# Kernel tuning notes

Measured on AMD Instinct MI355X. Metric: run time of the kernel, lower is better.

## Reference

```python
import jax, jax.numpy as jnp
import numpy as np
import itertools

LLR_MAX = 100.0


def _get_dist(llr, c_hat):
    # llr: [bs, n]; c_hat: [bs, cand, n] -> [bs, cand]
    # LLR-based distance from Stimming et al.: mean_n log(1 + exp(llr * (1 - 2c)))
    x = llr[:, None, :] * (1.0 - 2.0 * c_hat)
    return jnp.mean(jnp.log1p(jnp.exp(x)), axis=2)


def _int_mod_2(x):
    return jnp.mod(jnp.round(x), 2.0)


def _find_mrb(gm):
    # Batched GF(2) Gaussian elimination to most-reliable-basis.
    # gm: [bs, k, n] of 0/1 floats -> (gm_mrb [bs,k,n] systematic, idx_mrb [bs,n])
    bs, k, n = gm.shape

    def step(g, i):
        row = jax.lax.dynamic_slice_in_dim(g, i, 1, axis=1)[:, 0, :]   # [bs, n]
        p = jnp.argmax(row, axis=-1)                                   # first 1 -> pivot col, [bs]
        col = jnp.take_along_axis(g, p[:, None, None], axis=2)[:, :, 0]  # pivot column, [bs, k]
        col = col * (1.0 - jax.nn.one_hot(i, k, dtype=g.dtype))[None, :]  # don't eliminate row i itself
        g = jnp.mod(g + col[:, :, None] * row[:, None, :], 2.0)        # GF(2) row additions
        return g, p

    gm, pivots = jax.lax.scan(step, gm, jnp.arange(k))
    pivots = pivots.T.astype(jnp.int32)                                # [bs, k]
    # non-pivot columns, in original order, go to the back
    mark = jnp.zeros((bs, n), dtype=jnp.int32).at[jnp.arange(bs)[:, None], pivots].set(1)
    idx_parity = jnp.argsort(mark, axis=-1)[:, : n - k].astype(jnp.int32)  # stable: zeros (non-pivots) first
    idx_mrb = jnp.concatenate([pivots, idx_parity], axis=1)            # [bs, n]
    gm_mrb = jnp.take_along_axis(gm, idx_mrb[:, None, :], axis=2)      # systematic [I | P]
    return gm_mrb, idx_mrb


def _find_min_dist(llr, ep, gm_mrb, c):
    # ep: [P, t] error index patterns over the k MRB positions
    e = gm_mrb[:, ep, :]                       # [bs, P, t, n]
    e = jnp.sum(e, axis=2) + c[:, None, :]     # flip t rows of gm onto base codeword
    c_cand = _int_mod_2(e)                     # [bs, P, n]
    d = _get_dist(llr, c_cand)                 # [bs, P]
    idx = jnp.argmin(d, axis=1)
    c_hat = jnp.take_along_axis(c_cand, idx[:, None, None], axis=1)[:, 0, :]
    d_min = jnp.take_along_axis(d, idx[:, None], axis=1)[:, 0]
    return d_min, c_hat


def setup_inputs() -> dict:
    k, n, bs = 64, 128, 128
    rng = np.random.default_rng(0)
    # random systematic generator matrix [I_k | P] (already in the form make_systematic produces)
    P = rng.integers(0, 2, size=(k, n - k))
    gm = jnp.asarray(np.concatenate([np.eye(k, dtype=np.int64), P], axis=1), dtype=jnp.float32)
    key = jax.random.key(0)
    llrs_ch = 2.0 * jax.random.normal(key, (bs, n), dtype=jnp.float32)
    return {"llrs_ch": llrs_ch, "gm": gm, "t": 2}


def reference(llrs_ch, gm, t):
    llr = jnp.clip(llrs_ch, -LLR_MAX, LLR_MAX)
    bs, n = llr.shape
    k = gm.shape[0]
    # 1. sort by reliability |llr| (descending), permute gm columns identically
    idx_sort = jnp.argsort(-jnp.abs(llr), axis=-1).astype(jnp.int32)   # [bs, n]
    llr_sort = jnp.take_along_axis(llr, idx_sort, axis=1)
    gm_b = jnp.broadcast_to(gm[None], (bs, k, n))
    gm_sort = jnp.take_along_axis(gm_b, idx_sort[:, None, :], axis=2)
    # 2. most reliable basis via GF(2) Gaussian elimination
    gm_mrb, idx_mrb = _find_mrb(gm_sort)
    llr_mrb = jnp.take_along_axis(llr_sort, idx_mrb, axis=1)
    idx_total = jnp.take_along_axis(idx_sort, idx_mrb, axis=1)         # composed permutation
    # 3. hard-decide k most reliable bits and re-encode
    u_hat = (llr_mrb[:, :k] > 0.0).astype(llr.dtype)
    c = _int_mod_2(jnp.einsum('bk,bkn->bn', u_hat, gm_mrb))
    d_best = _get_dist(llr_mrb, c[:, None, :])[:, 0]
    c_best = c
    # 4. brute-force search over all error patterns with up to t flips
    for t_i in range(1, int(t) + 1):
        ep = jnp.asarray(list(itertools.combinations(range(k), t_i)), dtype=jnp.int32)
        d, c_hat = _find_min_dist(llr_mrb, ep, gm_mrb, c)
        better = d < d_best
        c_best = jnp.where(better[:, None], c_hat, c_best)
        d_best = jnp.where(better, d, d_best)
    # undo total column permutation
    idx_inv = jnp.argsort(idx_total, axis=-1)
    return jnp.take_along_axis(c_best, idx_inv, axis=1)
```

## Files before the change

kernel.cpp:

```cpp
#include <hip/hip_runtime.h>
#include <stdint.h>

#define K 64
#define N 128
#define BS 128
#define NPAIRS 2016
#define NCAND (64 + NPAIRS)
#define BLOCK 256

typedef unsigned long long u64;
typedef unsigned int u32;

__device__ inline u64 bcast64(u64 v, int lane) {
    int lo = __builtin_amdgcn_readlane((int)(u32)v, lane);
    int hi = __builtin_amdgcn_readlane((int)(u32)(v >> 32), lane);
    return ((u64)(u32)hi << 32) | (u32)lo;
}

__device__ inline int nth_set_bit(u64 m, int i) {
    int pos = 0;
#pragma unroll
    for (int w = 32; w >= 1; w >>= 1) {
        u64 mask = (1ull << w) - 1ull;
        int c = __popcll(m & mask);
        if (i >= c) { i -= c; m >>= w; pos += w; }
    }
    return pos;
}

__global__ __launch_bounds__(BLOCK) void osd_kernel(const float* __restrict__ llrs,
                                                    const float* __restrict__ gm,
                                                    float* __restrict__ out) {
    __shared__ float  lam[N];
    __shared__ u64    skey[N];
    __shared__ int    keyIdx[N];
    __shared__ float  lamSort[N];
    __shared__ u64    gmcols[N];
    __shared__ u64    cols[N];
    __shared__ int    pivotsLds[K];
    __shared__ int    idxpLds[K];
    __shared__ int    markLds[N];
    __shared__ u64    PmaskLds[K];
    __shared__ float  absMrb[K];
    __shared__ double sigLds[K];
    __shared__ double table[8 * 256];
    __shared__ double redS[4];
    __shared__ int    redId[4];
    __shared__ u64    cScal[4];

    const int tid = threadIdx.x;
    const int item = blockIdx.x;
    const float* llr = llrs + item * N;

    if (tid < N) {
        float v = llr[tid];
        v = fminf(fmaxf(v, -100.0f), 100.0f);
        lam[tid] = v;
        u32 ab = __float_as_uint(fabsf(v));
        skey[tid] = ((u64)(0xFFFFFFFFu - ab) << 32) | (u32)tid;
    }
    {
        int col = tid & 127, rh = tid >> 7;
        u32 w = 0;
#pragma unroll
        for (int i = 0; i < 32; ++i)
            w |= (u32)(gm[(rh * 32 + i) * N + col] != 0.0f) << i;
        ((u32*)gmcols)[col * 2 + rh] = w;
    }
    __syncthreads();

    if (tid < 64) {
        for (int k2 = 2; k2 <= N; k2 <<= 1) {
            for (int j = k2 >> 1; j >= 1; j >>= 1) {
                int i = ((tid & ~(j - 1)) << 1) | (tid & (j - 1));
                int ip = i | j;
                u64 a = skey[i], b = skey[ip];
                bool asc = ((i & k2) == 0);
                bool sw = asc ? (a > b) : (a < b);
                if (sw) { skey[i] = b; skey[ip] = a; }
            }
        }
        {
            u64 kv = skey[tid];      int ix = (int)(u32)kv;
            keyIdx[tid] = ix;        lamSort[tid] = lam[ix];
            kv = skey[tid + 64];     ix = (int)(u32)kv;
            keyIdx[tid + 64] = ix;   lamSort[tid + 64] = lam[ix];
        }

        u64 c0 = gmcols[keyIdx[tid]];
        u64 c1 = gmcols[keyIdx[tid + 64]];
        int pivotReg = 0;
        for (int i = 0; i < K; ++i) {
            int b0 = (int)((c0 >> i) & 1ull);
            int b1 = (int)((c1 >> i) & 1ull);
            u64 m0 = __ballot(b0);
            u64 m1 = __ballot(b1);
            int p = m0 ? __builtin_ctzll(m0) : (m1 ? 64 + __builtin_ctzll(m1) : 0);
            u64 colp = (p < 64) ? bcast64(c0, p & 63) : bcast64(c1, p & 63);
            u64 msk = colp & ~(1ull << i);
            if (b0) c0 ^= msk;
            if (b1) c1 ^= msk;
            pivotReg = (i == tid) ? p : pivotReg;
        }
        cols[tid] = c0;
        cols[tid + 64] = c1;
        pivotsLds[tid] = pivotReg;

        markLds[tid] = 0; markLds[tid + 64] = 0;
        markLds[pivotReg] = 1;
        u64 pm0 = __ballot(markLds[tid] != 0);
        u64 pm1 = __ballot(markLds[tid + 64] != 0);
        u64 nm0 = ~pm0, nm1 = ~pm1;
        int c0n = __popcll(nm0);
        int idxpReg = (tid < c0n) ? nth_set_bit(nm0, tid)
                                  : 64 + nth_set_bit(nm1, tid - c0n);
        idxpLds[tid] = idxpReg;

        u64 cp = cols[idxpReg];
        u64 P = 0;
#pragma unroll
        for (int x = 0; x < 64; ++x) {
            u64 bx = __ballot((int)((cp >> x) & 1ull));
            P = (x == tid) ? bx : P;
        }
        PmaskLds[tid] = P;

        float lpv = lamSort[pivotReg];
        int uh = lpv > 0.0f;
        absMrb[tid] = fabsf(lpv);
        u64 cLo = __ballot(uh);
        u64 x = uh ? P : 0ull;
#pragma unroll
        for (int off = 32; off >= 1; off >>= 1) x ^= __shfl_xor(x, off);
        u64 cHi = x;

        float lp = lamSort[idxpReg];
        int cbit = (int)((cHi >> tid) & 1ull);
        sigLds[tid] = cbit ? -(double)lp : (double)lp;

        if (tid == 0) { cScal[0] = cLo; cScal[1] = cHi; }
    }
    __syncthreads();

    {
        int pos = tid >> 5, grp = tid & 31;
        double sg[8];
#pragma unroll
        for (int j = 0; j < 8; ++j) sg[j] = sigLds[pos * 8 + j];
        int g = grp << 3;
        double base = 0.0;
#pragma unroll
        for (int j = 3; j < 8; ++j) if ((g >> j) & 1) base += sg[j];
#pragma unroll
        for (int e = 0; e < 8; ++e) {
            double s = base;
            if (e & 1) s += sg[0];
            if (e & 2) s += sg[1];
            if (e & 4) s += sg[2];
            table[pos * 256 + g + e] = s;
        }
    }
    __syncthreads();

    double bestS = 0.0; int bestId = 0;
    for (int c = tid; c < NCAND; c += BLOCK) {
        u64 mask; double pen; int id;
        if (c < 64) {
            mask = PmaskLds[c];
            pen = (double)absMrb[c];
            id = 1 + c;
        } else {
            int pid = c - 64;
            int lo = 0, hi = 62;
            while (lo < hi) {
                int mid = (lo + hi + 1) >> 1;
                int o = mid * 63 - ((mid * (mid - 1)) >> 1);
                if (o <= pid) lo = mid; else hi = mid - 1;
            }
            int a = lo;
            int oa = a * 63 - ((a * (a - 1)) >> 1);
            int b = a + 1 + (pid - oa);
            mask = PmaskLds[a] ^ PmaskLds[b];
            pen = (double)absMrb[a] + (double)absMrb[b];
            id = 65 + pid;
        }
        double W = 0.0;
#pragma unroll
        for (int p2 = 0; p2 < 8; ++p2)
            W += table[p2 * 256 + (int)((mask >> (p2 * 8)) & 255ull)];
        double s = W - pen;
        if (s > bestS || (s == bestS && id < bestId)) { bestS = s; bestId = id; }
    }
#pragma unroll
    for (int off = 32; off >= 1; off >>= 1) {
        double s2 = __shfl_xor(bestS, off);
        int i2 = __shfl_xor(bestId, off);
        if (s2 > bestS || (s2 == bestS && i2 < bestId)) { bestS = s2; bestId = i2; }
    }
    if ((tid & 63) == 0) { redS[tid >> 6] = bestS; redId[tid >> 6] = bestId; }
    __syncthreads();

    if (tid == 0) {
        double bS = redS[0]; int bi = redId[0];
        for (int w = 1; w < 4; ++w) {
            double s2 = redS[w]; int i2 = redId[w];
            if (s2 > bS || (s2 == bS && i2 < bi)) { bS = s2; bi = i2; }
        }
        u64 flo = 0, fhi = 0;
        if (bi >= 1 && bi <= 64) {
            int a = bi - 1; flo = 1ull << a; fhi = PmaskLds[a];
        } else if (bi >= 65) {
            int pid = bi - 65;
            int lo = 0, hi = 62;
            while (lo < hi) {
                int mid = (lo + hi + 1) >> 1;
                int o = mid * 63 - ((mid * (mid - 1)) >> 1);
                if (o <= pid) lo = mid; else hi = mid - 1;
            }
            int a = lo;
            int oa = a * 63 - ((a * (a - 1)) >> 1);
            int b = a + 1 + (pid - oa);
            flo = (1ull << a) | (1ull << b);
            fhi = PmaskLds[a] ^ PmaskLds[b];
        }
        cScal[2] = cScal[0] ^ flo;
        cScal[3] = cScal[1] ^ fhi;
    }
    __syncthreads();

    if (tid < N) {
        u64 cbLo = cScal[2], cbHi = cScal[3];
        int bit, mrbcol;
        if (tid < K) { bit = (int)((cbLo >> tid) & 1ull); mrbcol = pivotsLds[tid]; }
        else         { bit = (int)((cbHi >> (tid - K)) & 1ull); mrbcol = idxpLds[tid - K]; }
        out[item * N + keyIdx[mrbcol]] = (float)bit;
    }
}

extern "C" void kernel_launch(void* const* d_in, const int* in_sizes, int n_in,
                              void* d_out, int out_size, void* d_ws, size_t ws_size,
                              hipStream_t stream) {
    const float* llrs = (const float*)d_in[0];
    const float* gm   = (const float*)d_in[1];
    float* out = (float*)d_out;
    (void)in_sizes; (void)n_in; (void)out_size; (void)d_ws; (void)ws_size;
    osd_kernel<<<BS, BLOCK, 0, stream>>>(llrs, gm, out);
}
```

Baseline: 74.74 us.

## Replace bitonic sort with rank sort and streamline candidate scoring loop

Replaces the single-wave bitonic sort over 128 keys with a parallel rank-counting sort across 128 threads, where each thread counts the keys smaller than its own. The candidate loop is restructured: singles are handled by the first 64 threads, and pairs are handled in a fully unrolled loop with a branchless fixed-step binary search for pair decoding. The eight table lookups are also summed as a tree to shorten the dependency chain. This removes serialized sort stages and divergent while-loops, at the cost of O(N) LDS reads per thread in the rank sort and a different floating-point summation order.

```diff
diff --git a/kernel.cpp b/kernel.cpp
--- a/kernel.cpp
+++ b/kernel.cpp
@@ -5,7 +5,6 @@
 #define N 128
 #define BS 128
 #define NPAIRS 2016
-#define NCAND (64 + NPAIRS)
 #define BLOCK 256
 
 typedef unsigned long long u64;
@@ -26,6 +25,29 @@
         if (i >= c) { i -= c; m >>= w; pos += w; }
     }
     return pos;
+}
+
+__device__ inline double wsum(const double* __restrict__ table, u64 mask) {
+    double t0 = table[0 * 256 + (int)(mask & 255ull)];
+    double t1 = table[1 * 256 + (int)((mask >> 8) & 255ull)];
+    double t2 = table[2 * 256 + (int)((mask >> 16) & 255ull)];
+    double t3 = table[3 * 256 + (int)((mask >> 24) & 255ull)];
+    double t4 = table[4 * 256 + (int)((mask >> 32) & 255ull)];
+    double t5 = table[5 * 256 + (int)((mask >> 40) & 255ull)];
+    double t6 = table[6 * 256 + (int)((mask >> 48) & 255ull)];
+    double t7 = table[7 * 256 + (int)((mask >> 56) & 255ull)];
+    return ((t0 + t1) + (t2 + t3)) + ((t4 + t5) + (t6 + t7));
+}
+
+__device__ inline int pair_decode_a(int pid) {
+    int a = 0;
+#pragma unroll
+    for (int st = 32; st >= 1; st >>= 1) {
+        int cd = a + st;
+        int o = cd * 63 - ((cd * (cd - 1)) >> 1);
+        if (cd <= 62 && o <= pid) a = cd;
+    }
+    return a;
 }
 
 __global__ __launch_bounds__(BLOCK) void osd_kernel(const float* __restrict__ llrs,
@@ -69,24 +91,19 @@
     }
     __syncthreads();
 
+    if (tid < N) {
+        u64 myk = skey[tid];
+        int rank = 0;
+#pragma unroll 16
+        for (int j = 0; j < N; ++j)
+            rank += (int)(skey[j] < myk);
+        int ix = (int)(u32)myk;
+        keyIdx[rank] = ix;
+        lamSort[rank] = lam[ix];
+    }
+    __syncthreads();
+
     if (tid < 64) {
-        for (int k2 = 2; k2 <= N; k2 <<= 1) {
-            for (int j = k2 >> 1; j >= 1; j >>= 1) {
-                int i = ((tid & ~(j - 1)) << 1) | (tid & (j - 1));
-                int ip = i | j;
-                u64 a = skey[i], b = skey[ip];
-                bool asc = ((i & k2) == 0);
-                bool sw = asc ? (a > b) : (a < b);
-                if (sw) { skey[i] = b; skey[ip] = a; }
-            }
-        }
-        {
-            u64 kv = skey[tid];      int ix = (int)(u32)kv;
-            keyIdx[tid] = ix;        lamSort[tid] = lam[ix];
-            kv = skey[tid + 64];     ix = (int)(u32)kv;
-            keyIdx[tid + 64] = ix;   lamSort[tid + 64] = lam[ix];
-        }
-
         u64 c0 = gmcols[keyIdx[tid]];
         u64 c1 = gmcols[keyIdx[tid + 64]];
         int pivotReg = 0;
@@ -163,33 +180,22 @@
     __syncthreads();
 
     double bestS = 0.0; int bestId = 0;
-    for (int c = tid; c < NCAND; c += BLOCK) {
-        u64 mask; double pen; int id;
-        if (c < 64) {
-            mask = PmaskLds[c];
-            pen = (double)absMrb[c];
-            id = 1 + c;
-        } else {
-            int pid = c - 64;
-            int lo = 0, hi = 62;
-            while (lo < hi) {
-                int mid = (lo + hi + 1) >> 1;
-                int o = mid * 63 - ((mid * (mid - 1)) >> 1);
-                if (o <= pid) lo = mid; else hi = mid - 1;
-            }
-            int a = lo;
+    if (tid < 64) {
+        double s = wsum(table, PmaskLds[tid]) - (double)absMrb[tid];
+        if (s > bestS) { bestS = s; bestId = 1 + tid; }
+    }
+#pragma unroll
+    for (int it = 0; it < 8; ++it) {
+        int pid = tid + it * BLOCK;
+        if (pid < NPAIRS) {
+            int a = pair_decode_a(pid);
             int oa = a * 63 - ((a * (a - 1)) >> 1);
             int b = a + 1 + (pid - oa);
-            mask = PmaskLds[a] ^ PmaskLds[b];
-            pen = (double)absMrb[a] + (double)absMrb[b];
-            id = 65 + pid;
-        }
-        double W = 0.0;
-#pragma unroll
-        for (int p2 = 0; p2 < 8; ++p2)
-            W += table[p2 * 256 + (int)((mask >> (p2 * 8)) & 255ull)];
-        double s = W - pen;
-        if (s > bestS || (s == bestS && id < bestId)) { bestS = s; bestId = id; }
+            u64 mask = PmaskLds[a] ^ PmaskLds[b];
+            double s = wsum(table, mask) - (double)absMrb[a] - (double)absMrb[b];
+            int id = 65 + pid;
+            if (s > bestS || (s == bestS && id < bestId)) { bestS = s; bestId = id; }
+        }
     }
 #pragma unroll
     for (int off = 32; off >= 1; off >>= 1) {
@@ -211,13 +217,7 @@
             int a = bi - 1; flo = 1ull << a; fhi = PmaskLds[a];
         } else if (bi >= 65) {
             int pid = bi - 65;
-            int lo = 0, hi = 62;
-            while (lo < hi) {
-                int mid = (lo + hi + 1) >> 1;
-                int o = mid * 63 - ((mid * (mid - 1)) >> 1);
-                if (o <= pid) lo = mid; else hi = mid - 1;
-            }
-            int a = lo;
+            int a = pair_decode_a(pid);
             int oa = a * 63 - ((a * (a - 1)) >> 1);
             int b = a + 1 + (pid - oa);
             flo = (1ull << a) | (1ull << b);
```

Result: faster. 70.72 us (-5.4%).
